# Kernel tuning notes

Hardware: AMD Instinct MI355X
Metric: run time of the kernel (lower is better)

The kernel has to match this reference:

```python
import jax, jax.numpy as jnp
import numpy as np
import math

IN_DIM = 768
FREQ = IN_DIM // 2 + 1          # 385
K = max(1, int(FREQ * 0.1))     # 38
MLP_IN = 2 * K                  # 76
HID = 256
LN_EPS = 1e-5


def _spectral_mask(task_id=0):
    # Faithful port of PiNoiseBiLoRA._get_spectral_mask
    avail = np.arange(1, FREQ)
    mt = 20
    idx = avail[task_id % mt::mt]
    if len(idx) >= K:
        idx = idx[:K]
    else:
        needed = K - len(idx)
        rf = math.ceil(needed / len(idx))
        idx = np.concatenate([idx, np.tile(idx, rf)[:needed]])
    return idx.astype(np.int32)


def setup_inputs() -> dict:
    key = jax.random.key(0)
    ks = jax.random.split(key, 6)
    B, S = 8, 4096
    x = jax.random.normal(ks[0], (B, S, IN_DIM), dtype=jnp.float32)
    eps = jax.random.normal(ks[1], (B, S, MLP_IN), dtype=jnp.float32)
    indices = jnp.asarray(_spectral_mask(0))
    w_scale = 0.05
    mu_w1 = jax.random.normal(ks[2], (HID, MLP_IN), dtype=jnp.float32) * w_scale
    mu_w2 = jax.random.normal(ks[3], (MLP_IN, HID), dtype=jnp.float32) * w_scale
    sg_w1 = jax.random.normal(ks[4], (HID, MLP_IN), dtype=jnp.float32) * w_scale
    sg_w2 = jax.random.normal(ks[5], (MLP_IN, HID), dtype=jnp.float32) * w_scale
    zeros_h = jnp.zeros((HID,), jnp.float32)
    zeros_o = jnp.zeros((MLP_IN,), jnp.float32)
    ones_h = jnp.ones((HID,), jnp.float32)
    return {
        'x': x, 'eps': eps, 'indices': indices,
        'mu_w1': mu_w1, 'mu_b1': zeros_h, 'mu_g': ones_h, 'mu_beta': zeros_h,
        'mu_w2': mu_w2, 'mu_b2': zeros_o,
        'sg_w1': sg_w1, 'sg_b1': zeros_h, 'sg_g': ones_h, 'sg_beta': zeros_h,
        'sg_w2': sg_w2, 'sg_b2': zeros_o,
    }


def _mlp(x, w1, b1, g, beta, w2, b2):
    # Linear -> LayerNorm -> GELU(exact) -> Linear
    h = x @ w1.T + b1
    mu = h.mean(axis=-1, keepdims=True)
    var = jnp.mean((h - mu) ** 2, axis=-1, keepdims=True)
    h = (h - mu) * jax.lax.rsqrt(var + LN_EPS) * g + beta
    h = jax.nn.gelu(h, approximate=False)
    return h @ w2.T + b2


def reference(x, eps, indices,
              mu_w1, mu_b1, mu_g, mu_beta, mu_w2, mu_b2,
              sg_w1, sg_b1, sg_g, sg_beta, sg_w2, sg_b2):
    # Training-mode forward of PiNoiseBiLoRA
    x_freq = jnp.fft.rfft(x, axis=-1)            # [B,S,FREQ] complex64
    x_sel = x_freq[..., indices]                 # gather k freq bins
    x_in = jnp.concatenate([x_sel.real, x_sel.imag], axis=-1)  # [B,S,2k]
    mu = _mlp(x_in, mu_w1, mu_b1, mu_g, mu_beta, mu_w2, mu_b2)
    sigma = _mlp(x_in, sg_w1, sg_b1, sg_g, sg_beta, sg_w2, sg_b2)
    z = mu + eps * sigma                         # reparameterization
    z_complex = jax.lax.complex(z[..., :K], z[..., K:]).astype(jnp.complex64)
    noise = jnp.zeros(x_freq.shape, jnp.complex64).at[..., indices].add(z_complex)
    return jnp.fft.irfft(noise, n=IN_DIM, axis=-1)
```

## Files before the change

### kernel.cpp

```cpp
#include <hip/hip_runtime.h>
#include <hip/hip_bf16.h>
#include <math.h>

#define INDIM 768
#define NROWS 32768
#define KSEL  38
#define NCOLS 76
#define HID   256
#define LN_EPS 1e-5f

typedef float  f32x4  __attribute__((ext_vector_type(4)));
typedef __bf16 bf16x8 __attribute__((ext_vector_type(8)));

#define MFMA16(a,b,c) __builtin_amdgcn_mfma_f32_16x16x32_bf16((a),(b),(c),0,0,0)

#define OFF_BFP 0
#define OFF_W1P 122880
#define OFF_W2P 221184
#define OFF_BSP 303104

__global__ void k_prep(const int* __restrict__ idxs,
                       const float* __restrict__ mu_w1, const float* __restrict__ sg_w1,
                       const float* __restrict__ mu_w2, const float* __restrict__ sg_w2,
                       __bf16* __restrict__ BfP, __bf16* __restrict__ W1P,
                       __bf16* __restrict__ W2P, __bf16* __restrict__ BsP)
{
    int tid = blockIdx.x * blockDim.x + threadIdx.x;
    int nth = gridDim.x * blockDim.x;
    const float TH = 6.28318530717958647692f / (float)INDIM;

    for (int e = tid; e < 120 * 512; e += nth) {
        int frag = e >> 9, lane = (e >> 3) & 63, j = e & 7;
        int kc = frag / 5, nt = frag % 5;
        int c = nt * 16 + (lane & 15);
        int k = kc * 32 + ((lane >> 4) << 3) + j;
        float v = 0.f;
        if (c < NCOLS) {
            int cc = (c < KSEL) ? c : c - KSEL;
            int f = idxs[cc];
            int m = (f * k) % INDIM;
            float s, co; sincosf(TH * (float)m, &s, &co);
            v = (c < KSEL) ? co : -s;
        }
        BfP[e] = (__bf16)v;
    }
    for (int e = tid; e < 96 * 512; e += nth) {
        int frag = e >> 9, lane = (e >> 3) & 63, j = e & 7;
        int mlp = frag / 48; int r = frag % 48;
        int nt = r / 3, ks = r % 3;
        int row = nt * 16 + (lane & 15);
        int k = ks * 32 + ((lane >> 4) << 3) + j;
        const float* W = mlp ? sg_w1 : mu_w1;
        W1P[e] = (__bf16)((k < NCOLS) ? W[row * NCOLS + k] : 0.f);
    }
    for (int e = tid; e < 80 * 512; e += nth) {
        int frag = e >> 9, lane = (e >> 3) & 63, j = e & 7;
        int mlp = frag / 40; int r = frag % 40;
        int nt = r / 8, ks = r % 8;
        int row = nt * 16 + (lane & 15);
        int k = ks * 32 + ((lane >> 4) << 3) + j;
        const float* W = mlp ? sg_w2 : mu_w2;
        W2P[e] = (__bf16)((row < NCOLS) ? W[row * HID + k] : 0.f);
    }
    for (int e = tid; e < 144 * 512; e += nth) {
        int frag = e >> 9, lane = (e >> 3) & 63, j = e & 7;
        int nt = frag / 3, ks = frag % 3;
        int n = nt * 16 + (lane & 15);
        int k = ks * 32 + ((lane >> 4) << 3) + j;
        float v = 0.f;
        if (k < NCOLS) {
            int cc = (k < KSEL) ? k : k - KSEL;
            int f = idxs[cc];
            int m = (f * n) % INDIM;
            float s, co; sincosf(TH * (float)m, &s, &co);
            v = ((k < KSEL) ? co : -s) * (2.0f / (float)INDIM);
        }
        BsP[e] = (__bf16)v;
    }
}

static __device__ inline float gelu_fast(float v) {
    float u = v * (0.79788456080286535588f + 0.03567740813636141f * v * v);
    return v / (1.f + __expf(-2.f * u));
}

__global__ __launch_bounds__(256, 4) void k_fused(
    const float* __restrict__ x, const float* __restrict__ eps,
    const __bf16* __restrict__ Bf, const __bf16* __restrict__ W1f,
    const __bf16* __restrict__ W2f, const __bf16* __restrict__ Bs,
    const float* __restrict__ mu_b1, const float* __restrict__ mu_g,
    const float* __restrict__ mu_be, const float* __restrict__ mu_b2,
    const float* __restrict__ sg_b1, const float* __restrict__ sg_g,
    const float* __restrict__ sg_be, const float* __restrict__ sg_b2,
    float* __restrict__ out)
{
    __shared__ __bf16 tbuf[2][1664];
    __shared__ char   ureg[17408];
    float*  PA = (float*)ureg;
    __bf16* GW = (__bf16*)ureg;

    int tid = threadIdx.x;
    int w = tid >> 6, lane = tid & 63, q = lane >> 4, l16 = lane & 15;
    int t = w >> 1, p = w & 1;
    int rbase = blockIdx.x * 32 + t * 16;

    f32x4 acc[5] = {};
    {
        const float* xrow = x + (size_t)(rbase + l16) * INDIM + p * 384 + q * 8;
        #pragma unroll
        for (int kk = 0; kk < 12; ++kk) {
            int kc = p * 12 + kk;
            float4 f0 = ((const float4*)(xrow + kk * 32))[0];
            float4 f1 = ((const float4*)(xrow + kk * 32))[1];
            union { __bf16 h[8]; bf16x8 v; } a;
            a.h[0]=(__bf16)f0.x; a.h[1]=(__bf16)f0.y; a.h[2]=(__bf16)f0.z; a.h[3]=(__bf16)f0.w;
            a.h[4]=(__bf16)f1.x; a.h[5]=(__bf16)f1.y; a.h[6]=(__bf16)f1.z; a.h[7]=(__bf16)f1.w;
            #pragma unroll
            for (int nt = 0; nt < 5; ++nt) {
                bf16x8 b = *(const bf16x8*)&Bf[(size_t)((kc * 5 + nt) * 64 + lane) * 8];
                acc[nt] = MFMA16(a.v, b, acc[nt]);
            }
        }
    }
    if (p == 1) {
        #pragma unroll
        for (int nt = 0; nt < 5; ++nt)
            #pragma unroll
            for (int r = 0; r < 4; ++r)
                PA[t * 1280 + (q * 4 + r) * 80 + nt * 16 + l16] = acc[nt][r];
    }
    __syncthreads();
    if (p == 0) {
        #pragma unroll
        for (int nt = 0; nt < 5; ++nt)
            #pragma unroll
            for (int r = 0; r < 4; ++r) {
                float v = acc[nt][r] + PA[t * 1280 + (q * 4 + r) * 80 + nt * 16 + l16];
                tbuf[t][(q * 4 + r) * 104 + nt * 16 + l16] = (__bf16)v;
            }
        #pragma unroll
        for (int r = 0; r < 4; ++r)
            tbuf[t][(q * 4 + r) * 104 + 80 + l16] = (__bf16)0.f;
    }
    __syncthreads();
    bf16x8 a1[3];
    #pragma unroll
    for (int ks = 0; ks < 3; ++ks)
        a1[ks] = *(const bf16x8*)&tbuf[t][l16 * 104 + ks * 32 + q * 8];

    const float* b1 = p ? sg_b1 : mu_b1;
    const float* g  = p ? sg_g  : mu_g;
    const float* be = p ? sg_be : mu_be;

    f32x4 h[16] = {};
    #pragma unroll
    for (int nt = 0; nt < 16; ++nt)
        #pragma unroll
        for (int ks = 0; ks < 3; ++ks) {
            bf16x8 b = *(const bf16x8*)&W1f[(size_t)((p * 48 + nt * 3 + ks) * 64 + lane) * 8];
            h[nt] = MFMA16(a1[ks], b, h[nt]);
        }
    float s[4] = {}, ss[4] = {};
    #pragma unroll
    for (int nt = 0; nt < 16; ++nt) {
        float bb = b1[nt * 16 + l16];
        #pragma unroll
        for (int r = 0; r < 4; ++r) {
            float v = h[nt][r] + bb; h[nt][r] = v;
            s[r] += v; ss[r] += v * v;
        }
    }
    #pragma unroll
    for (int off = 1; off < 16; off <<= 1)
        #pragma unroll
        for (int r = 0; r < 4; ++r) {
            s[r] += __shfl_xor(s[r], off); ss[r] += __shfl_xor(ss[r], off);
        }
    float mean[4], rstd[4];
    #pragma unroll
    for (int r = 0; r < 4; ++r) {
        mean[r] = s[r] * (1.f / 256.f);
        rstd[r] = rsqrtf(ss[r] * (1.f / 256.f) - mean[r] * mean[r] + LN_EPS);
    }
    __bf16* gw = &GW[w * 2176];
    bf16x8 a2[8];
    #pragma unroll
    for (int half = 0; half < 2; ++half) {
        #pragma unroll
        for (int ntl = 0; ntl < 8; ++ntl) {
            int nt = half * 8 + ntl;
            int i = nt * 16 + l16;
            float gv = g[i], bev = be[i];
            #pragma unroll
            for (int r = 0; r < 4; ++r)
                gw[(q * 4 + r) * 136 + ntl * 16 + l16] =
                    (__bf16)gelu_fast((h[nt][r] - mean[r]) * rstd[r] * gv + bev);
        }
        #pragma unroll
        for (int ks = 0; ks < 4; ++ks)
            a2[half * 4 + ks] = *(const bf16x8*)&gw[l16 * 136 + ks * 32 + q * 8];
    }

    f32x4 o[5] = {};
    #pragma unroll
    for (int nt = 0; nt < 5; ++nt)
        #pragma unroll
        for (int ks = 0; ks < 8; ++ks) {
            bf16x8 b = *(const bf16x8*)&W2f[(size_t)((p * 40 + nt * 8 + ks) * 64 + lane) * 8];
            o[nt] = MFMA16(a2[ks], b, o[nt]);
        }

    __syncthreads();
    float ev[5][4];
    if (p == 0) {
        #pragma unroll
        for (int nt = 0; nt < 5; ++nt)
            #pragma unroll
            for (int r = 0; r < 4; ++r)
                PA[t * 1280 + (q * 4 + r) * 80 + nt * 16 + l16] = o[nt][r];
    } else {
        #pragma unroll
        for (int nt = 0; nt < 5; ++nt) {
            int j = nt * 16 + l16;
            #pragma unroll
            for (int r = 0; r < 4; ++r)
                ev[nt][r] = (j < NCOLS)
                    ? eps[(size_t)(rbase + q * 4 + r) * NCOLS + j] : 0.f;
        }
    }
    __syncthreads();
    if (p == 1) {
        #pragma unroll
        for (int nt = 0; nt < 5; ++nt) {
            int j = nt * 16 + l16;
            float b2m = (j < NCOLS) ? mu_b2[j] : 0.f;
            float b2s = (j < NCOLS) ? sg_b2[j] : 0.f;
            #pragma unroll
            for (int r = 0; r < 4; ++r) {
                float z = 0.f;
                if (j < NCOLS) {
                    float omu = PA[t * 1280 + (q * 4 + r) * 80 + j];
                    z = (omu + b2m) + ev[nt][r] * (o[nt][r] + b2s);
                }
                tbuf[t][(q * 4 + r) * 104 + j] = (__bf16)z;
            }
        }
        #pragma unroll
        for (int r = 0; r < 4; ++r)
            tbuf[t][(q * 4 + r) * 104 + 80 + l16] = (__bf16)0.f;
    }
    __syncthreads();
    bf16x8 az[3];
    #pragma unroll
    for (int ks = 0; ks < 3; ++ks)
        az[ks] = *(const bf16x8*)&tbuf[t][l16 * 104 + ks * 32 + q * 8];

    #pragma unroll 6
    for (int k = 0; k < 24; ++k) {
        int nt = p * 24 + k;
        f32x4 oc = {};
        #pragma unroll
        for (int ks = 0; ks < 3; ++ks) {
            bf16x8 b = *(const bf16x8*)&Bs[(size_t)((nt * 3 + ks) * 64 + lane) * 8];
            oc = MFMA16(az[ks], b, oc);
        }
        #pragma unroll
        for (int r = 0; r < 4; ++r)
            out[(size_t)(rbase + q * 4 + r) * INDIM + nt * 16 + l16] = oc[r];
    }
}

extern "C" void kernel_launch(void* const* d_in, const int* in_sizes, int n_in,
                              void* d_out, int out_size, void* d_ws, size_t ws_size,
                              hipStream_t stream)
{
    const float* x     = (const float*)d_in[0];
    const float* eps   = (const float*)d_in[1];
    const int*   idxs  = (const int*)  d_in[2];
    const float* mu_w1 = (const float*)d_in[3];
    const float* mu_b1 = (const float*)d_in[4];
    const float* mu_g  = (const float*)d_in[5];
    const float* mu_be = (const float*)d_in[6];
    const float* mu_w2 = (const float*)d_in[7];
    const float* mu_b2 = (const float*)d_in[8];
    const float* sg_w1 = (const float*)d_in[9];
    const float* sg_b1 = (const float*)d_in[10];
    const float* sg_g  = (const float*)d_in[11];
    const float* sg_be = (const float*)d_in[12];
    const float* sg_w2 = (const float*)d_in[13];
    const float* sg_b2 = (const float*)d_in[14];
    float* out = (float*)d_out;

    char* ws = (char*)d_ws;
    __bf16* BfP = (__bf16*)(ws + OFF_BFP);
    __bf16* W1P = (__bf16*)(ws + OFF_W1P);
    __bf16* W2P = (__bf16*)(ws + OFF_W2P);
    __bf16* BsP = (__bf16*)(ws + OFF_BSP);

    hipLaunchKernelGGL(k_prep, dim3(1024), dim3(256), 0, stream,
                       idxs, mu_w1, sg_w1, mu_w2, sg_w2, BfP, W1P, W2P, BsP);
    hipLaunchKernelGGL(k_fused, dim3(NROWS / 32), dim3(256), 0, stream,
                       x, eps, BfP, W1P, W2P, BsP,
                       mu_b1, mu_g, mu_be, mu_b2,
                       sg_b1, sg_g, sg_be, sg_b2, out);
}
```

Before: 247.8 us.

## Double-buffer weight fragments into LDS via global_load_lds across all GEMM stages

Every wave used to read bf16 weight fragments (DFT basis, W1, W2, inverse basis) straight from global memory. Each GEMM stage now stages the next chunk of weights into a double-buffered LDS region with async global_load_lds, while the MFMAs run on the current chunk. The x row loads are also software-prefetched one step ahead. This adds many block-wide barriers per stage and enlarges shared memory from about 17 KB to about 24 KB, which may hurt occupancy at 4 blocks per CU and serialise waves on the syncs.

```diff
diff --git a/kernel.cpp b/kernel.cpp
--- a/kernel.cpp
+++ b/kernel.cpp
@@ -84,6 +84,19 @@
     return v / (1.f + __expf(-2.f * u));
 }
 
+static __device__ __forceinline__ void stage_runs(
+    const __bf16* __restrict__ s0, const __bf16* __restrict__ s1,
+    int nkb, char* dst, int w, int lane)
+{
+    typedef __attribute__((address_space(1))) const unsigned int g_u32;
+    typedef __attribute__((address_space(3))) unsigned int l_u32;
+    for (int u = w; u < 2 * nkb; u += 4) {
+        const __bf16* s = (u < nkb) ? (s0 + u * 512) : (s1 + (u - nkb) * 512);
+        __builtin_amdgcn_global_load_lds((g_u32*)(s + lane * 8),
+                                         (l_u32*)(dst + u * 1024), 16, 0, 0);
+    }
+}
+
 __global__ __launch_bounds__(256, 4) void k_fused(
     const float* __restrict__ x, const float* __restrict__ eps,
     const __bf16* __restrict__ Bf, const __bf16* __restrict__ W1f,
@@ -94,10 +107,10 @@
     const float* __restrict__ sg_be, const float* __restrict__ sg_b2,
     float* __restrict__ out)
 {
-    __shared__ __bf16 tbuf[2][1664];
-    __shared__ char   ureg[17408];
-    float*  PA = (float*)ureg;
-    __bf16* GW = (__bf16*)ureg;
+    __shared__ __align__(16) __bf16 tbuf[2][1664];
+    __shared__ __align__(16) char   R[24576];
+    float*  PA = (float*)R;
+    __bf16* GW = (__bf16*)R;
 
     int tid = threadIdx.x;
     int w = tid >> 6, lane = tid & 63, q = lane >> 4, l16 = lane & 15;
@@ -107,19 +120,32 @@
     f32x4 acc[5] = {};
     {
         const float* xrow = x + (size_t)(rbase + l16) * INDIM + p * 384 + q * 8;
+        stage_runs(Bf, Bf + (size_t)60 * 512, 5, R, w, lane);
+        float4 f0 = ((const float4*)xrow)[0];
+        float4 f1 = ((const float4*)xrow)[1];
+        __syncthreads();
         #pragma unroll
         for (int kk = 0; kk < 12; ++kk) {
-            int kc = p * 12 + kk;
-            float4 f0 = ((const float4*)(xrow + kk * 32))[0];
-            float4 f1 = ((const float4*)(xrow + kk * 32))[1];
+            int buf = kk & 1;
+            float4 n0, n1;
+            if (kk < 11) {
+                stage_runs(Bf + (size_t)(kk + 1) * 5 * 512,
+                           Bf + (size_t)(13 + kk) * 5 * 512,
+                           5, R + (buf ^ 1) * 10240, w, lane);
+                n0 = ((const float4*)(xrow + (kk + 1) * 32))[0];
+                n1 = ((const float4*)(xrow + (kk + 1) * 32))[1];
+            }
             union { __bf16 h[8]; bf16x8 v; } a;
             a.h[0]=(__bf16)f0.x; a.h[1]=(__bf16)f0.y; a.h[2]=(__bf16)f0.z; a.h[3]=(__bf16)f0.w;
             a.h[4]=(__bf16)f1.x; a.h[5]=(__bf16)f1.y; a.h[6]=(__bf16)f1.z; a.h[7]=(__bf16)f1.w;
+            const char* bb = R + buf * 10240 + p * 5120 + (size_t)lane * 16;
             #pragma unroll
             for (int nt = 0; nt < 5; ++nt) {
-                bf16x8 b = *(const bf16x8*)&Bf[(size_t)((kc * 5 + nt) * 64 + lane) * 8];
+                bf16x8 b = *(const bf16x8*)(bb + nt * 1024);
                 acc[nt] = MFMA16(a.v, b, acc[nt]);
             }
+            __syncthreads();
+            if (kk < 11) { f0 = n0; f1 = n1; }
         }
     }
     if (p == 1) {
@@ -152,14 +178,28 @@
     const float* g  = p ? sg_g  : mu_g;
     const float* be = p ? sg_be : mu_be;
 
+    stage_runs(W1f, W1f + (size_t)48 * 512, 6, R, w, lane);
+    __syncthreads();
     f32x4 h[16] = {};
     #pragma unroll
-    for (int nt = 0; nt < 16; ++nt)
-        #pragma unroll
-        for (int ks = 0; ks < 3; ++ks) {
-            bf16x8 b = *(const bf16x8*)&W1f[(size_t)((p * 48 + nt * 3 + ks) * 64 + lane) * 8];
-            h[nt] = MFMA16(a1[ks], b, h[nt]);
-        }
+    for (int c = 0; c < 8; ++c) {
+        int buf = c & 1;
+        if (c < 7)
+            stage_runs(W1f + (size_t)(6 * (c + 1)) * 512,
+                       W1f + (size_t)(48 + 6 * (c + 1)) * 512,
+                       6, R + (buf ^ 1) * 12288, w, lane);
+        const char* bb = R + buf * 12288 + p * 6144 + (size_t)lane * 16;
+        #pragma unroll
+        for (int ntl = 0; ntl < 2; ++ntl) {
+            int nt = 2 * c + ntl;
+            #pragma unroll
+            for (int ks = 0; ks < 3; ++ks) {
+                bf16x8 b = *(const bf16x8*)(bb + (ntl * 3 + ks) * 1024);
+                h[nt] = MFMA16(a1[ks], b, h[nt]);
+            }
+        }
+        __syncthreads();
+    }
     float s[4] = {}, ss[4] = {};
     #pragma unroll
     for (int nt = 0; nt < 16; ++nt) {
@@ -200,17 +240,30 @@
         for (int ks = 0; ks < 4; ++ks)
             a2[half * 4 + ks] = *(const bf16x8*)&gw[l16 * 136 + ks * 32 + q * 8];
     }
-
+    __syncthreads();
+
+    stage_runs(W2f, W2f + (size_t)40 * 512, 4, R, w, lane);
+    __syncthreads();
     f32x4 o[5] = {};
     #pragma unroll
-    for (int nt = 0; nt < 5; ++nt)
-        #pragma unroll
-        for (int ks = 0; ks < 8; ++ks) {
-            bf16x8 b = *(const bf16x8*)&W2f[(size_t)((p * 40 + nt * 8 + ks) * 64 + lane) * 8];
-            o[nt] = MFMA16(a2[ks], b, o[nt]);
-        }
-
-    __syncthreads();
+    for (int c = 0; c < 10; ++c) {
+        int buf = c & 1;
+        if (c < 9) {
+            int nn = (c + 1) >> 1, hf = (c + 1) & 1;
+            stage_runs(W2f + (size_t)(nn * 8 + hf * 4) * 512,
+                       W2f + (size_t)(40 + nn * 8 + hf * 4) * 512,
+                       4, R + (buf ^ 1) * 8192, w, lane);
+        }
+        int nt = c >> 1, hf = c & 1;
+        const char* bb = R + buf * 8192 + p * 4096 + (size_t)lane * 16;
+        #pragma unroll
+        for (int k4 = 0; k4 < 4; ++k4) {
+            bf16x8 b = *(const bf16x8*)(bb + k4 * 1024);
+            o[nt] = MFMA16(a2[hf * 4 + k4], b, o[nt]);
+        }
+        __syncthreads();
+    }
+
     float ev[5][4];
     if (p == 0) {
         #pragma unroll
@@ -254,19 +307,31 @@
     #pragma unroll
     for (int ks = 0; ks < 3; ++ks)
         az[ks] = *(const bf16x8*)&tbuf[t][l16 * 104 + ks * 32 + q * 8];
-
-    #pragma unroll 6
-    for (int k = 0; k < 24; ++k) {
-        int nt = p * 24 + k;
-        f32x4 oc = {};
-        #pragma unroll
-        for (int ks = 0; ks < 3; ++ks) {
-            bf16x8 b = *(const bf16x8*)&Bs[(size_t)((nt * 3 + ks) * 64 + lane) * 8];
-            oc = MFMA16(az[ks], b, oc);
-        }
-        #pragma unroll
-        for (int r = 0; r < 4; ++r)
-            out[(size_t)(rbase + q * 4 + r) * INDIM + nt * 16 + l16] = oc[r];
+    stage_runs(Bs, Bs + (size_t)72 * 512, 6, R, w, lane);
+    __syncthreads();
+
+    #pragma unroll
+    for (int c = 0; c < 12; ++c) {
+        int buf = c & 1;
+        if (c < 11)
+            stage_runs(Bs + (size_t)(6 * (c + 1)) * 512,
+                       Bs + (size_t)(72 + 6 * (c + 1)) * 512,
+                       6, R + (buf ^ 1) * 12288, w, lane);
+        const char* bb = R + buf * 12288 + p * 6144 + (size_t)lane * 16;
+        #pragma unroll
+        for (int kloc = 0; kloc < 2; ++kloc) {
+            int nt = p * 24 + 2 * c + kloc;
+            f32x4 oc = {};
+            #pragma unroll
+            for (int ks = 0; ks < 3; ++ks) {
+                bf16x8 b = *(const bf16x8*)(bb + (kloc * 3 + ks) * 1024);
+                oc = MFMA16(az[ks], b, oc);
+            }
+            #pragma unroll
+            for (int r = 0; r < 4; ++r)
+                out[(size_t)(rbase + q * 4 + r) * INDIM + nt * 16 + l16] = oc[r];
+        }
+        if (c < 11) __syncthreads();
     }
 }
 
```

Result: faster. 240.1 us (-3.1%).

## Stage weight tiles into LDS via async global_load_lds with 1024-thread blocks

Applied to the files above, without the earlier changes.

Blocks grow from 256 to 1024 threads, so each block handles 128 rows. Each weight matrix (DFT basis, W1, W2, inverse basis) is staged once per block into a 120KB LDS region using global_load_lds, so the MFMA B operands come from LDS instead of each wave reading them from global/L2. The x row loads are also prefetched one iteration ahead in the forward-DFT loop. The cost is many more block-wide barriers across 16 waves and a very large LDS footprint, which limits each CU to a single resident block.

```diff
diff --git a/kernel.cpp b/kernel.cpp
--- a/kernel.cpp
+++ b/kernel.cpp
@@ -84,7 +84,17 @@
     return v / (1.f + __expf(-2.f * u));
 }
 
-__global__ __launch_bounds__(256, 4) void k_fused(
+static __device__ __forceinline__ void stage16(
+    const __bf16* __restrict__ src, int nunits, char* dst, int w, int lane)
+{
+    typedef __attribute__((address_space(1))) const unsigned int g_u32;
+    typedef __attribute__((address_space(3))) unsigned int l_u32;
+    for (int u = w; u < nunits; u += 16)
+        __builtin_amdgcn_global_load_lds((g_u32*)(src + (size_t)u * 512 + lane * 8),
+                                         (l_u32*)(dst + u * 1024), 16, 0, 0);
+}
+
+__global__ __launch_bounds__(1024, 4) void k_fused(
     const float* __restrict__ x, const float* __restrict__ eps,
     const __bf16* __restrict__ Bf, const __bf16* __restrict__ W1f,
     const __bf16* __restrict__ W2f, const __bf16* __restrict__ Bs,
@@ -94,34 +104,42 @@
     const float* __restrict__ sg_be, const float* __restrict__ sg_b2,
     float* __restrict__ out)
 {
-    __shared__ __bf16 tbuf[2][1664];
-    __shared__ char   ureg[17408];
-    float*  PA = (float*)ureg;
-    __bf16* GW = (__bf16*)ureg;
+    __shared__ __align__(16) char   R[122880];
+    __shared__ __align__(16) __bf16 tbuf[8][1664];
+    float* PA = (float*)R;
 
     int tid = threadIdx.x;
     int w = tid >> 6, lane = tid & 63, q = lane >> 4, l16 = lane & 15;
     int t = w >> 1, p = w & 1;
-    int rbase = blockIdx.x * 32 + t * 16;
+    int rbase = blockIdx.x * 128 + t * 16;
 
     f32x4 acc[5] = {};
     {
         const float* xrow = x + (size_t)(rbase + l16) * INDIM + p * 384 + q * 8;
+        stage16(Bf, 120, R, w, lane);
+        float4 f0 = ((const float4*)xrow)[0];
+        float4 f1 = ((const float4*)xrow)[1];
+        __syncthreads();
         #pragma unroll
         for (int kk = 0; kk < 12; ++kk) {
-            int kc = p * 12 + kk;
-            float4 f0 = ((const float4*)(xrow + kk * 32))[0];
-            float4 f1 = ((const float4*)(xrow + kk * 32))[1];
+            float4 n0, n1;
+            if (kk < 11) {
+                n0 = ((const float4*)(xrow + (kk + 1) * 32))[0];
+                n1 = ((const float4*)(xrow + (kk + 1) * 32))[1];
+            }
             union { __bf16 h[8]; bf16x8 v; } a;
             a.h[0]=(__bf16)f0.x; a.h[1]=(__bf16)f0.y; a.h[2]=(__bf16)f0.z; a.h[3]=(__bf16)f0.w;
             a.h[4]=(__bf16)f1.x; a.h[5]=(__bf16)f1.y; a.h[6]=(__bf16)f1.z; a.h[7]=(__bf16)f1.w;
+            const char* bb = R + (size_t)((p * 12 + kk) * 5) * 1024 + (size_t)lane * 16;
             #pragma unroll
             for (int nt = 0; nt < 5; ++nt) {
-                bf16x8 b = *(const bf16x8*)&Bf[(size_t)((kc * 5 + nt) * 64 + lane) * 8];
+                bf16x8 b = *(const bf16x8*)(bb + nt * 1024);
                 acc[nt] = MFMA16(a.v, b, acc[nt]);
             }
-        }
-    }
+            if (kk < 11) { f0 = n0; f1 = n1; }
+        }
+    }
+    __syncthreads();
     if (p == 1) {
         #pragma unroll
         for (int nt = 0; nt < 5; ++nt)
@@ -147,6 +165,8 @@
     #pragma unroll
     for (int ks = 0; ks < 3; ++ks)
         a1[ks] = *(const bf16x8*)&tbuf[t][l16 * 104 + ks * 32 + q * 8];
+    stage16(W1f, 96, R, w, lane);
+    __syncthreads();
 
     const float* b1 = p ? sg_b1 : mu_b1;
     const float* g  = p ? sg_g  : mu_g;
@@ -157,7 +177,8 @@
     for (int nt = 0; nt < 16; ++nt)
         #pragma unroll
         for (int ks = 0; ks < 3; ++ks) {
-            bf16x8 b = *(const bf16x8*)&W1f[(size_t)((p * 48 + nt * 3 + ks) * 64 + lane) * 8];
+            bf16x8 b = *(const bf16x8*)(R + (size_t)((p * 48 + nt * 3 + ks) * 1024)
+                                          + (size_t)lane * 16);
             h[nt] = MFMA16(a1[ks], b, h[nt]);
         }
     float s[4] = {}, ss[4] = {};
@@ -182,7 +203,8 @@
         mean[r] = s[r] * (1.f / 256.f);
         rstd[r] = rsqrtf(ss[r] * (1.f / 256.f) - mean[r] * mean[r] + LN_EPS);
     }
-    __bf16* gw = &GW[w * 2176];
+    __syncthreads();
+    __bf16* gw = (__bf16*)R + w * 2176;
     bf16x8 a2[8];
     #pragma unroll
     for (int half = 0; half < 2; ++half) {
@@ -200,17 +222,21 @@
         for (int ks = 0; ks < 4; ++ks)
             a2[half * 4 + ks] = *(const bf16x8*)&gw[l16 * 136 + ks * 32 + q * 8];
     }
+    __syncthreads();
+    stage16(W2f, 80, R, w, lane);
+    __syncthreads();
 
     f32x4 o[5] = {};
     #pragma unroll
     for (int nt = 0; nt < 5; ++nt)
         #pragma unroll
         for (int ks = 0; ks < 8; ++ks) {
-            bf16x8 b = *(const bf16x8*)&W2f[(size_t)((p * 40 + nt * 8 + ks) * 64 + lane) * 8];
+            bf16x8 b = *(const bf16x8*)(R + (size_t)((p * 40 + nt * 8 + ks) * 1024)
+                                          + (size_t)lane * 16);
             o[nt] = MFMA16(a2[ks], b, o[nt]);
         }
-
-    __syncthreads();
+    __syncthreads();
+
     float ev[5][4];
     if (p == 0) {
         #pragma unroll
@@ -254,19 +280,31 @@
     #pragma unroll
     for (int ks = 0; ks < 3; ++ks)
         az[ks] = *(const bf16x8*)&tbuf[t][l16 * 104 + ks * 32 + q * 8];
-
-    #pragma unroll 6
-    for (int k = 0; k < 24; ++k) {
-        int nt = p * 24 + k;
-        f32x4 oc = {};
-        #pragma unroll
-        for (int ks = 0; ks < 3; ++ks) {
-            bf16x8 b = *(const bf16x8*)&Bs[(size_t)((nt * 3 + ks) * 64 + lane) * 8];
-            oc = MFMA16(az[ks], b, oc);
-        }
-        #pragma unroll
-        for (int r = 0; r < 4; ++r)
-            out[(size_t)(rbase + q * 4 + r) * INDIM + nt * 16 + l16] = oc[r];
+    stage16(Bs, 72, R, w, lane);
+    __syncthreads();
+
+    #pragma unroll
+    for (int half = 0; half < 2; ++half) {
+        if (half == 1) {
+            __syncthreads();
+            stage16(Bs + (size_t)72 * 512, 72, R, w, lane);
+            __syncthreads();
+        }
+        #pragma unroll 4
+        for (int c = 0; c < 12; ++c) {
+            int ntl = p * 12 + c;
+            int nt  = half * 24 + ntl;
+            f32x4 oc = {};
+            #pragma unroll
+            for (int ks = 0; ks < 3; ++ks) {
+                bf16x8 b = *(const bf16x8*)(R + (size_t)((ntl * 3 + ks) * 1024)
+                                              + (size_t)lane * 16);
+                oc = MFMA16(az[ks], b, oc);
+            }
+            #pragma unroll
+            for (int r = 0; r < 4; ++r)
+                out[(size_t)(rbase + q * 4 + r) * INDIM + nt * 16 + l16] = oc[r];
+        }
     }
 }
 
@@ -299,7 +337,7 @@
 
     hipLaunchKernelGGL(k_prep, dim3(1024), dim3(256), 0, stream,
                        idxs, mu_w1, sg_w1, mu_w2, sg_w2, BfP, W1P, W2P, BsP);
-    hipLaunchKernelGGL(k_fused, dim3(NROWS / 32), dim3(256), 0, stream,
+    hipLaunchKernelGGL(k_fused, dim3(NROWS / 128), dim3(1024), 0, stream,
                        x, eps, BfP, W1P, W2P, BsP,
                        mu_b1, mu_g, mu_be, mu_b2,
                        sg_b1, sg_g, sg_be, sg_b2, out);
```

Result: faster. 235.7 us (-4.9%).

## Split fused kernel into DFT, MLP, and synthesis kernels via bf16 workspace

Applied to the files above, without the earlier changes.

Breaks the single fused kernel into three launches: a forward-DFT GEMM kernel writing bf16 spectral features to a workspace, an MLP kernel that reads them and writes the bf16 latent z, and a synthesis GEMM kernel that writes the output. Each stage gets its own parallel split (the DFT and synthesis kernels use 16-row blocks with a 4-way K or N split and higher occupancy bounds), so the light DFT and synthesis stages are not held to the register-heavy MLP's occupancy. In exchange it adds two kernel launches and round-trips small intermediates (about 6 MB each) through global memory. The workspace offsets must fit within the provided workspace size.

```diff
diff --git a/kernel.cpp b/kernel.cpp
--- a/kernel.cpp
+++ b/kernel.cpp
@@ -18,6 +18,8 @@
 #define OFF_W1P 122880
 #define OFF_W2P 221184
 #define OFF_BSP 303104
+#define OFF_Z1  450560
+#define OFF_Z2  6742016
 
 __global__ void k_prep(const int* __restrict__ idxs,
                        const float* __restrict__ mu_w1, const float* __restrict__ sg_w1,
@@ -84,80 +86,86 @@
     return v / (1.f + __expf(-2.f * u));
 }
 
-__global__ __launch_bounds__(256, 4) void k_fused(
-    const float* __restrict__ x, const float* __restrict__ eps,
-    const __bf16* __restrict__ Bf, const __bf16* __restrict__ W1f,
-    const __bf16* __restrict__ W2f, const __bf16* __restrict__ Bs,
+__global__ __launch_bounds__(256, 8) void k_dft(
+    const float* __restrict__ x, const __bf16* __restrict__ Bf,
+    __bf16* __restrict__ z1)
+{
+    __shared__ __align__(16) float PA[3][1280];
+    int tid = threadIdx.x;
+    int w = tid >> 6, lane = tid & 63, q = lane >> 4, l16 = lane & 15;
+    int rbase = blockIdx.x * 16;
+
+    f32x4 acc[5] = {};
+    const float* xrow = x + (size_t)(rbase + l16) * INDIM + w * 192 + q * 8;
+    const __bf16* bfb = Bf + (size_t)(w * 30) * 512 + (size_t)lane * 8;
+    #pragma unroll
+    for (int kk = 0; kk < 6; ++kk) {
+        float4 f0 = ((const float4*)(xrow + kk * 32))[0];
+        float4 f1 = ((const float4*)(xrow + kk * 32))[1];
+        union { __bf16 h[8]; bf16x8 v; } a;
+        a.h[0]=(__bf16)f0.x; a.h[1]=(__bf16)f0.y; a.h[2]=(__bf16)f0.z; a.h[3]=(__bf16)f0.w;
+        a.h[4]=(__bf16)f1.x; a.h[5]=(__bf16)f1.y; a.h[6]=(__bf16)f1.z; a.h[7]=(__bf16)f1.w;
+        #pragma unroll
+        for (int nt = 0; nt < 5; ++nt) {
+            bf16x8 b = *(const bf16x8*)(bfb + (size_t)(kk * 5 + nt) * 512);
+            acc[nt] = MFMA16(a.v, b, acc[nt]);
+        }
+    }
+    if (w > 0) {
+        #pragma unroll
+        for (int nt = 0; nt < 5; ++nt)
+            #pragma unroll
+            for (int r = 0; r < 4; ++r)
+                PA[w - 1][(q * 4 + r) * 80 + nt * 16 + l16] = acc[nt][r];
+    }
+    __syncthreads();
+    if (w == 0) {
+        #pragma unroll
+        for (int nt = 0; nt < 5; ++nt)
+            #pragma unroll
+            for (int r = 0; r < 4; ++r) {
+                int i = (q * 4 + r) * 80 + nt * 16 + l16;
+                float v = acc[nt][r] + PA[0][i] + PA[1][i] + PA[2][i];
+                z1[(size_t)(rbase + q * 4 + r) * 96 + nt * 16 + l16] = (__bf16)v;
+            }
+        #pragma unroll
+        for (int r = 0; r < 4; ++r)
+            ((unsigned short*)z1)[(size_t)(rbase + q * 4 + r) * 96 + 80 + l16] = 0;
+    }
+}
+
+__global__ __launch_bounds__(256, 4) void k_mlp(
+    const __bf16* __restrict__ z1, const float* __restrict__ eps,
+    const __bf16* __restrict__ W1f, const __bf16* __restrict__ W2f,
     const float* __restrict__ mu_b1, const float* __restrict__ mu_g,
     const float* __restrict__ mu_be, const float* __restrict__ mu_b2,
     const float* __restrict__ sg_b1, const float* __restrict__ sg_g,
     const float* __restrict__ sg_be, const float* __restrict__ sg_b2,
-    float* __restrict__ out)
-{
-    __shared__ __bf16 tbuf[2][1664];
-    __shared__ char   ureg[17408];
-    float*  PA = (float*)ureg;
-    __bf16* GW = (__bf16*)ureg;
-
+    __bf16* __restrict__ z2)
+{
+    __shared__ __align__(16) float  PA[2][1280];
+    __shared__ __align__(16) __bf16 GW[4][2176];
     int tid = threadIdx.x;
     int w = tid >> 6, lane = tid & 63, q = lane >> 4, l16 = lane & 15;
     int t = w >> 1, p = w & 1;
     int rbase = blockIdx.x * 32 + t * 16;
 
-    f32x4 acc[5] = {};
-    {
-        const float* xrow = x + (size_t)(rbase + l16) * INDIM + p * 384 + q * 8;
-        #pragma unroll
-        for (int kk = 0; kk < 12; ++kk) {
-            int kc = p * 12 + kk;
-            float4 f0 = ((const float4*)(xrow + kk * 32))[0];
-            float4 f1 = ((const float4*)(xrow + kk * 32))[1];
-            union { __bf16 h[8]; bf16x8 v; } a;
-            a.h[0]=(__bf16)f0.x; a.h[1]=(__bf16)f0.y; a.h[2]=(__bf16)f0.z; a.h[3]=(__bf16)f0.w;
-            a.h[4]=(__bf16)f1.x; a.h[5]=(__bf16)f1.y; a.h[6]=(__bf16)f1.z; a.h[7]=(__bf16)f1.w;
-            #pragma unroll
-            for (int nt = 0; nt < 5; ++nt) {
-                bf16x8 b = *(const bf16x8*)&Bf[(size_t)((kc * 5 + nt) * 64 + lane) * 8];
-                acc[nt] = MFMA16(a.v, b, acc[nt]);
-            }
-        }
-    }
-    if (p == 1) {
-        #pragma unroll
-        for (int nt = 0; nt < 5; ++nt)
-            #pragma unroll
-            for (int r = 0; r < 4; ++r)
-                PA[t * 1280 + (q * 4 + r) * 80 + nt * 16 + l16] = acc[nt][r];
-    }
-    __syncthreads();
-    if (p == 0) {
-        #pragma unroll
-        for (int nt = 0; nt < 5; ++nt)
-            #pragma unroll
-            for (int r = 0; r < 4; ++r) {
-                float v = acc[nt][r] + PA[t * 1280 + (q * 4 + r) * 80 + nt * 16 + l16];
-                tbuf[t][(q * 4 + r) * 104 + nt * 16 + l16] = (__bf16)v;
-            }
-        #pragma unroll
-        for (int r = 0; r < 4; ++r)
-            tbuf[t][(q * 4 + r) * 104 + 80 + l16] = (__bf16)0.f;
-    }
-    __syncthreads();
     bf16x8 a1[3];
     #pragma unroll
     for (int ks = 0; ks < 3; ++ks)
-        a1[ks] = *(const bf16x8*)&tbuf[t][l16 * 104 + ks * 32 + q * 8];
+        a1[ks] = *(const bf16x8*)(z1 + (size_t)(rbase + l16) * 96 + ks * 32 + q * 8);
 
     const float* b1 = p ? sg_b1 : mu_b1;
     const float* g  = p ? sg_g  : mu_g;
     const float* be = p ? sg_be : mu_be;
 
+    const __bf16* w1b = W1f + (size_t)(p * 48) * 512 + (size_t)lane * 8;
     f32x4 h[16] = {};
     #pragma unroll
     for (int nt = 0; nt < 16; ++nt)
         #pragma unroll
         for (int ks = 0; ks < 3; ++ks) {
-            bf16x8 b = *(const bf16x8*)&W1f[(size_t)((p * 48 + nt * 3 + ks) * 64 + lane) * 8];
+            bf16x8 b = *(const bf16x8*)(w1b + (size_t)(nt * 3 + ks) * 512);
             h[nt] = MFMA16(a1[ks], b, h[nt]);
         }
     float s[4] = {}, ss[4] = {};
@@ -182,7 +190,7 @@
         mean[r] = s[r] * (1.f / 256.f);
         rstd[r] = rsqrtf(ss[r] * (1.f / 256.f) - mean[r] * mean[r] + LN_EPS);
     }
-    __bf16* gw = &GW[w * 2176];
+    __bf16* gw = &GW[w][0];
     bf16x8 a2[8];
     #pragma unroll
     for (int half = 0; half < 2; ++half) {
@@ -200,24 +208,22 @@
         for (int ks = 0; ks < 4; ++ks)
             a2[half * 4 + ks] = *(const bf16x8*)&gw[l16 * 136 + ks * 32 + q * 8];
     }
-
+    const __bf16* w2b = W2f + (size_t)(p * 40) * 512 + (size_t)lane * 8;
     f32x4 o[5] = {};
     #pragma unroll
     for (int nt = 0; nt < 5; ++nt)
         #pragma unroll
         for (int ks = 0; ks < 8; ++ks) {
-            bf16x8 b = *(const bf16x8*)&W2f[(size_t)((p * 40 + nt * 8 + ks) * 64 + lane) * 8];
+            bf16x8 b = *(const bf16x8*)(w2b + (size_t)(nt * 8 + ks) * 512);
             o[nt] = MFMA16(a2[ks], b, o[nt]);
         }
-
-    __syncthreads();
     float ev[5][4];
     if (p == 0) {
         #pragma unroll
         for (int nt = 0; nt < 5; ++nt)
             #pragma unroll
             for (int r = 0; r < 4; ++r)
-                PA[t * 1280 + (q * 4 + r) * 80 + nt * 16 + l16] = o[nt][r];
+                PA[t][(q * 4 + r) * 80 + nt * 16 + l16] = o[nt][r];
     } else {
         #pragma unroll
         for (int nt = 0; nt < 5; ++nt) {
@@ -239,34 +245,43 @@
             for (int r = 0; r < 4; ++r) {
                 float z = 0.f;
                 if (j < NCOLS) {
-                    float omu = PA[t * 1280 + (q * 4 + r) * 80 + j];
+                    float omu = PA[t][(q * 4 + r) * 80 + j];
                     z = (omu + b2m) + ev[nt][r] * (o[nt][r] + b2s);
                 }
-                tbuf[t][(q * 4 + r) * 104 + j] = (__bf16)z;
+                z2[(size_t)(rbase + q * 4 + r) * 96 + j] = (__bf16)z;
             }
         }
         #pragma unroll
         for (int r = 0; r < 4; ++r)
-            tbuf[t][(q * 4 + r) * 104 + 80 + l16] = (__bf16)0.f;
-    }
-    __syncthreads();
+            ((unsigned short*)z2)[(size_t)(rbase + q * 4 + r) * 96 + 80 + l16] = 0;
+    }
+}
+
+__global__ __launch_bounds__(256, 8) void k_syn(
+    const __bf16* __restrict__ z2, const __bf16* __restrict__ Bs,
+    float* __restrict__ out)
+{
+    int tid = threadIdx.x;
+    int w = tid >> 6, lane = tid & 63, q = lane >> 4, l16 = lane & 15;
+    int rbase = blockIdx.x * 16;
+
     bf16x8 az[3];
     #pragma unroll
     for (int ks = 0; ks < 3; ++ks)
-        az[ks] = *(const bf16x8*)&tbuf[t][l16 * 104 + ks * 32 + q * 8];
-
-    #pragma unroll 6
-    for (int k = 0; k < 24; ++k) {
-        int nt = p * 24 + k;
+        az[ks] = *(const bf16x8*)(z2 + (size_t)(rbase + l16) * 96 + ks * 32 + q * 8);
+
+    const __bf16* bsb = Bs + (size_t)(w * 36) * 512 + (size_t)lane * 8;
+    #pragma unroll 4
+    for (int ntl = 0; ntl < 12; ++ntl) {
         f32x4 oc = {};
         #pragma unroll
         for (int ks = 0; ks < 3; ++ks) {
-            bf16x8 b = *(const bf16x8*)&Bs[(size_t)((nt * 3 + ks) * 64 + lane) * 8];
+            bf16x8 b = *(const bf16x8*)(bsb + (size_t)(ntl * 3 + ks) * 512);
             oc = MFMA16(az[ks], b, oc);
         }
         #pragma unroll
         for (int r = 0; r < 4; ++r)
-            out[(size_t)(rbase + q * 4 + r) * INDIM + nt * 16 + l16] = oc[r];
+            out[(size_t)(rbase + q * 4 + r) * INDIM + w * 192 + ntl * 16 + l16] = oc[r];
     }
 }
 
@@ -296,11 +311,17 @@
     __bf16* W1P = (__bf16*)(ws + OFF_W1P);
     __bf16* W2P = (__bf16*)(ws + OFF_W2P);
     __bf16* BsP = (__bf16*)(ws + OFF_BSP);
+    __bf16* Z1  = (__bf16*)(ws + OFF_Z1);
+    __bf16* Z2  = (__bf16*)(ws + OFF_Z2);
 
     hipLaunchKernelGGL(k_prep, dim3(1024), dim3(256), 0, stream,
                        idxs, mu_w1, sg_w1, mu_w2, sg_w2, BfP, W1P, W2P, BsP);
-    hipLaunchKernelGGL(k_fused, dim3(NROWS / 32), dim3(256), 0, stream,
-                       x, eps, BfP, W1P, W2P, BsP,
+    hipLaunchKernelGGL(k_dft, dim3(NROWS / 16), dim3(256), 0, stream,
+                       x, BfP, Z1);
+    hipLaunchKernelGGL(k_mlp, dim3(NROWS / 32), dim3(256), 0, stream,
+                       Z1, eps, W1P, W2P,
                        mu_b1, mu_g, mu_be, mu_b2,
-                       sg_b1, sg_g, sg_be, sg_b2, out);
-}
+                       sg_b1, sg_g, sg_be, sg_b2, Z2);
+    hipLaunchKernelGGL(k_syn, dim3(NROWS / 16), dim3(256), 0, stream,
+                       Z2, BsP, out);
+}
```

Measured after the change: 252.7 us. Within noise of the previous version (+2.0%).
